# Performance work log

Measured on AMD Instinct MI355X. Metric: run time of the kernel, lower is better.

## Reference

```python
import jax, jax.numpy as jnp
import numpy as np

B, S, E, D, H = 4, 2048, 512, 64, 8
NEG = float(np.finfo(np.float64).min)  # tf uses tf.float64.min; overflows to -inf in fp32, same softmax effect


def setup_inputs() -> dict:
    key = jax.random.key(0)
    ks = jax.random.split(key, 6)
    std = 0.05  # tf.random_normal_initializer default stddev
    x = jax.random.normal(ks[0], (B, S, E), dtype=jnp.float32)
    Wq = jax.random.normal(ks[1], (H, E, D), dtype=jnp.float32) * std
    Wk = jax.random.normal(ks[2], (H, E, D), dtype=jnp.float32) * std
    Wvd = jax.random.normal(ks[3], (H, E, D), dtype=jnp.float32) * std
    Wvu = jax.random.normal(ks[4], (H, D, E), dtype=jnp.float32) * std
    Wo = jax.random.normal(ks[5], (H, 1), dtype=jnp.float32) * std
    return {"x": x, "Wq": Wq, "Wk": Wk, "Wvd": Wvd, "Wvu": Wvu, "Wo": Wo}


def reference(x, Wq, Wk, Wvd, Wvu, Wo):
    # Per-head projections, vectorized over the head axis h
    Q = jnp.einsum("bse,hed->bhsd", x, Wq)  # [B,H,S,D]
    K = jnp.einsum("bse,hed->bhsd", x, Wk)
    score = jnp.einsum("bhsd,bhtd->bhst", Q, K) / jnp.sqrt(jnp.float32(D))
    # tf.linalg.band_part(score, -1, 0): keep lower triangle (causal)
    tril = jnp.tril(jnp.ones((S, S), dtype=bool))
    score = jnp.where(tril, score, 0.0)
    # tf.where(score != 0, score, float64.min): masks zeros (incl. any exact-zero kept entries)
    score = jnp.where(score != 0, score, jnp.float32(NEG))
    attn = jax.nn.softmax(score, axis=-1)  # [B,H,S,S]
    # low-rank value projection: x @ (Wvdown @ Wvup) per head
    Wv = jnp.einsum("hed,hdf->hef", Wvd, Wvu)  # [H,E,E]
    V = jnp.einsum("bse,hef->bhsf", x, Wv)      # [B,H,S,E]
    heads = jnp.einsum("bhst,bhte->bhse", attn, V)  # [B,H,S,E]
    # stack on last axis then matmul with Wo[H,1] == weighted sum over heads
    out = jnp.einsum("bhse,h->bse", heads, Wo[:, 0])
    return out
```

## Files before the change

### kernel.cpp

```cpp
#include <hip/hip_runtime.h>
#include <math.h>
#include <type_traits>

namespace {
constexpr int B = 4, S = 2048, E = 512, D = 64, H = 8;
constexpr int KD = 512;

typedef short bf8 __attribute__((ext_vector_type(8)));
typedef short bf4 __attribute__((ext_vector_type(4)));
typedef float f4 __attribute__((ext_vector_type(4)));

__device__ __forceinline__ short f2bf(float f) {
  union { float f; unsigned u; } v; v.f = f;
  const unsigned r = v.u + 0x7fffu + ((v.u >> 16) & 1u);
  return (short)(r >> 16);
}

__device__ __forceinline__ unsigned cvt_pk_bf16(float a, float b) {
  unsigned r;
  asm("v_cvt_pk_bf16_f32 %0, %1, %2" : "=v"(r) : "v"(a), "v"(b));
  return r;
}

__device__ __forceinline__ void gload16(const void* g, void* l) {
  __builtin_amdgcn_global_load_lds(
      (const __attribute__((address_space(1))) unsigned int*)g,
      (__attribute__((address_space(3))) unsigned int*)l, 16, 0, 0);
}

__global__ __launch_bounds__(256) void prep_kernel(
    const float* __restrict__ x, const float* __restrict__ Wq,
    const float* __restrict__ Wk, const float* __restrict__ Wvd,
    const float* __restrict__ Wvu, const float* __restrict__ Wo,
    short* __restrict__ xb, short* __restrict__ WcatT,
    short* __restrict__ W2T) {
  __shared__ float T[64][65];
  const int bid = blockIdx.x;
  const int tid = threadIdx.x;
  if (bid < 2048) {
    const size_t i = ((size_t)bid * 256 + tid) * 8;
    const float4 v0 = *(const float4*)(x + i);
    const float4 v1 = *(const float4*)(x + i + 4);
    bf8 o;
    o[0] = f2bf(v0.x); o[1] = f2bf(v0.y); o[2] = f2bf(v0.z); o[3] = f2bf(v0.w);
    o[4] = f2bf(v1.x); o[5] = f2bf(v1.y); o[6] = f2bf(v1.z); o[7] = f2bf(v1.w);
    *(bf8*)(xb + i) = o;
  } else if (bid < 2240) {
    const int r = bid - 2048;
    const int cb = r >> 3, e0 = (r & 7) * 64;
    const int w = cb >> 3, h = cb & 7;
    const float* Wsel = (w == 0) ? Wq : (w == 1) ? Wk : Wvd;
    const float* Wp = Wsel + (size_t)h * E * D;
#pragma unroll
    for (int i = 0; i < 4; ++i) {
      const int f = tid + i * 256;
      const int rr = f >> 4, c4 = f & 15;
      const float4 v = *(const float4*)(Wp + (size_t)(e0 + rr) * D + c4 * 4);
      T[rr][c4 * 4 + 0] = v.x; T[rr][c4 * 4 + 1] = v.y;
      T[rr][c4 * 4 + 2] = v.z; T[rr][c4 * 4 + 3] = v.w;
    }
    __syncthreads();
#pragma unroll
    for (int i = 0; i < 4; ++i) {
      const int f = tid + i * 256;
      const int dr = f >> 4, e4 = f & 15;
      bf4 o;
#pragma unroll
      for (int j = 0; j < 4; ++j) o[j] = f2bf(T[e4 * 4 + j][dr]);
      *(bf4*)(WcatT + (size_t)(cb * 64 + dr) * KD + e0 + e4 * 4) = o;
    }
  } else {
    const int r = bid - 2240;
    const int h = r >> 3, e0 = (r & 7) * 64;
    const float wo = Wo[h];
#pragma unroll
    for (int i = 0; i < 4; ++i) {
      const int f = tid + i * 256;
      const int rr = f >> 4, c4 = f & 15;
      const float4 v = *(const float4*)(Wvu + ((size_t)h * D + rr) * E + e0 + c4 * 4);
      T[rr][c4 * 4 + 0] = v.x * wo; T[rr][c4 * 4 + 1] = v.y * wo;
      T[rr][c4 * 4 + 2] = v.z * wo; T[rr][c4 * 4 + 3] = v.w * wo;
    }
    __syncthreads();
#pragma unroll
    for (int i = 0; i < 4; ++i) {
      const int f = tid + i * 256;
      const int er = f >> 4, d4 = f & 15;
      bf4 o;
#pragma unroll
      for (int j = 0; j < 4; ++j) o[j] = f2bf(T[d4 * 4 + j][er]);
      *(bf4*)(W2T + (size_t)(e0 + er) * KD + h * 64 + d4 * 4) = o;
    }
  }
}

template <int MODE>
__global__ __launch_bounds__(256) void gemm_kernel(
    const short* __restrict__ A, const short* __restrict__ Bt,
    short* __restrict__ Qb, short* __restrict__ Kb, short* __restrict__ Vtg,
    float* __restrict__ Of) {
  const int row0 = blockIdx.x * 128;
  const int ct = blockIdx.y;
  const int tid = threadIdx.x;
  const int w = tid >> 6, l = tid & 63;
  const int wm = w >> 1, wn = w & 1;
  const int lr = l & 15, hi = l >> 4;

  __shared__ short As[128 * 64];
  __shared__ short Bs[128 * 64];

  const short* Ag = A + (size_t)row0 * KD;
  const short* Bg = Bt + (size_t)ct * 128 * KD;

  f4 acc[4][4] = {};
  for (int k0 = 0; k0 < KD; k0 += 64) {
    __syncthreads();
#pragma unroll
    for (int i = 0; i < 4; ++i) {
      const int f = i * 256 + tid;
      const int r = f >> 3, g = f & 7;
      gload16(Ag + (size_t)r * KD + k0 + ((g ^ (r & 7)) << 3), &As[f * 8]);
    }
#pragma unroll
    for (int i = 0; i < 4; ++i) {
      const int f = i * 256 + tid;
      const int r = f >> 3, g = f & 7;
      gload16(Bg + (size_t)r * KD + k0 + ((g ^ (r & 7)) << 3), &Bs[f * 8]);
    }
    __syncthreads();

    bf8 af[4][2], bfv[4][2];
#pragma unroll
    for (int t = 0; t < 4; ++t) {
#pragma unroll
      for (int kh = 0; kh < 2; ++kh) {
        const int ar = wm * 64 + t * 16 + lr;
        af[t][kh] = *(const bf8*)&As[ar * 64 + (((kh * 4 + hi) ^ (ar & 7)) << 3)];
        const int br = wn * 64 + t * 16 + lr;
        bfv[t][kh] = *(const bf8*)&Bs[br * 64 + (((kh * 4 + hi) ^ (br & 7)) << 3)];
      }
    }
#pragma unroll
    for (int mt = 0; mt < 4; ++mt)
#pragma unroll
      for (int nt = 0; nt < 4; ++nt) {
        acc[mt][nt] =
            __builtin_amdgcn_mfma_f32_16x16x32_bf16(af[mt][0], bfv[nt][0], acc[mt][nt], 0, 0, 0);
        acc[mt][nt] =
            __builtin_amdgcn_mfma_f32_16x16x32_bf16(af[mt][1], bfv[nt][1], acc[mt][nt], 0, 0, 0);
      }
  }

  if constexpr (MODE == 0) {
#pragma unroll
    for (int nt = 0; nt < 4; ++nt) {
      const int gc = ct * 128 + wn * 64 + nt * 16 + lr;
      const int cb = gc >> 6, d = gc & 63;
      const int h = cb & 7;
      if (cb < 16) {
        short* Out = (cb < 8) ? Qb : Kb;
#pragma unroll
        for (int mt = 0; mt < 4; ++mt)
#pragma unroll
          for (int reg = 0; reg < 4; ++reg) {
            const int grow = row0 + wm * 64 + mt * 16 + hi * 4 + reg;
            const int b = grow >> 11, s = grow & (S - 1);
            Out[(((size_t)(b * H + h) * S + s) << 6) + d] = f2bf(acc[mt][nt][reg]);
          }
      } else {
        const int hswap = ((d >> 3) & 1) << 2;
#pragma unroll
        for (int mt = 0; mt < 4; ++mt) {
          const int grow0 = row0 + wm * 64 + mt * 16 + hi * 4;
          const int b = grow0 >> 11, s0 = (grow0 & (S - 1)) ^ hswap;
          bf4 o;
#pragma unroll
          for (int reg = 0; reg < 4; ++reg) o[reg] = f2bf(acc[mt][nt][reg]);
          *(bf4*)(Vtg + (((size_t)(b * H + h) * D + d) << 11) + s0) = o;
        }
      }
    }
  } else {
#pragma unroll
    for (int mt = 0; mt < 4; ++mt)
#pragma unroll
      for (int reg = 0; reg < 4; ++reg) {
        const int grow = row0 + wm * 64 + mt * 16 + hi * 4 + reg;
        float* orow = Of + (size_t)grow * 512 + ct * 128 + wn * 64;
#pragma unroll
        for (int nt = 0; nt < 4; ++nt) orow[nt * 16 + lr] = acc[mt][nt][reg];
      }
  }
}

__global__ __launch_bounds__(256) void attn_kernel(
    const short* __restrict__ Qb, const short* __restrict__ Kb,
    const short* __restrict__ Vt, short* __restrict__ PVb) {
  const int bh = blockIdx.x;
  const int j = blockIdx.y;
  const int qtA = j, qtB = 31 - j;
  const int nA = j + 1;
  const int b = bh >> 3, h = bh & 7;
  const int tid = threadIdx.x;
  const int w = tid >> 6, l = tid & 63;
  const int lr = l & 15, hi = l >> 4;

  __shared__ short Ks[2][64 * 64];
  __shared__ short Vs[2][64 * 64];

  const short* QgA = Qb + ((size_t)bh * S + qtA * 64 + w * 16 + lr) * D;
  const short* QgB = Qb + ((size_t)bh * S + qtB * 64 + w * 16 + lr) * D;
  const bf8 qA0 = *(const bf8*)(QgA + hi * 8);
  const bf8 qA1 = *(const bf8*)(QgA + 32 + hi * 8);
  const bf8 qB0 = *(const bf8*)(QgB + hi * 8);
  const bf8 qB1 = *(const bf8*)(QgB + 32 + hi * 8);

  const short* Kg = Kb + (size_t)bh * S * D;
  const short* Vg = Vt + (size_t)bh * D * S;

  const int sr = tid >> 3, sg = tid & 7;
  const int sswz = (sg ^ (sr & 7)) << 3;
  const int sr2 = sr + 32, sswz2 = (sg ^ (sr2 & 7)) << 3;
  const short* kg0 = Kg + (size_t)sr * D + sswz;
  const short* kg1 = Kg + (size_t)sr2 * D + sswz2;
  const short* vg0 = Vg + (size_t)sr * S + sswz;
  const short* vg1 = Vg + (size_t)sr2 * S + sswz2;

  const int e7 = lr & 7;
  const int kla0 = lr * 128 + ((hi ^ e7) << 4);
  const int kla1 = kla0 ^ 64;
  const int x7 = (hi >> 1) ^ e7;
  const int swaph = ((hi & 1) ^ ((lr >> 3) & 1)) << 3;
  int vla[4];
#pragma unroll
  for (int np = 0; np < 4; ++np)
    vla[np] = lr * 128 + (((2 * np) ^ x7) << 4) + swaph;

  float lsum4[4] = {};
  f4 accO[4] = {};

  auto step = [&](int buf, bf8 q0, bf8 q1, auto diag_c) {
    constexpr bool DIAG = decltype(diag_c)::value;
    const char* Klb = (const char*)Ks[buf];
    const char* Vlb = (const char*)Vs[buf];
    f4 accS[4] = {};
    __builtin_amdgcn_s_setprio(1);
#pragma unroll
    for (int n = 0; n < 4; ++n) {
      const bf8 k0 = *(const bf8*)(Klb + kla0 + n * 2048);
      const bf8 k1 = *(const bf8*)(Klb + kla1 + n * 2048);
      accS[n] = __builtin_amdgcn_mfma_f32_16x16x32_bf16(k0, q0, accS[n], 0, 0, 0);
      accS[n] = __builtin_amdgcn_mfma_f32_16x16x32_bf16(k1, q1, accS[n], 0, 0, 0);
    }
    __builtin_amdgcn_s_setprio(0);

    bf4 pa[4];
#pragma unroll
    for (int n = 0; n < 4; ++n) {
      float p[4];
#pragma unroll
      for (int reg = 0; reg < 4; ++reg) {
        float pv = __expf(fmaf(accS[n][reg], 0.125f, -12.0f));
        if constexpr (DIAG) {
          const bool ok = (n * 16 + hi * 4 + reg) <= (w * 16 + lr);
          pv = ok ? pv : 0.f;
        }
        p[reg] = pv;
        lsum4[reg] += pv;
      }
      union { int2 i; bf4 v; } u;
      u.i.x = (int)cvt_pk_bf16(p[0], p[1]);
      u.i.y = (int)cvt_pk_bf16(p[2], p[3]);
      pa[n] = u.v;
    }

    __builtin_amdgcn_s_setprio(1);
#pragma unroll
    for (int np = 0; np < 4; ++np) {
#pragma unroll
      for (int ne = 0; ne < 4; ++ne) {
        const bf4 vf = *(const bf4*)(Vlb + vla[np] + ne * 2048);
        accO[ne] = __builtin_amdgcn_mfma_f32_16x16x16bf16_1k(pa[np], vf, accO[ne], 0, 0, 0);
      }
    }
    __builtin_amdgcn_s_setprio(0);
  };

  auto epi = [&](int qt) {
    float lv = (lsum4[0] + lsum4[1]) + (lsum4[2] + lsum4[3]);
    lv += __shfl_xor(lv, 16);
    lv += __shfl_xor(lv, 32);
#pragma unroll
    for (int reg = 0; reg < 4; ++reg) {
      const float lq = __shfl(lv, hi * 4 + reg);
      const float inv = 1.f / lq;
      const int s = qt * 64 + w * 16 + hi * 4 + reg;
      short* op = PVb + (size_t)(b * S + s) * (H * D) + h * D;
#pragma unroll
      for (int n = 0; n < 4; ++n) op[n * 16 + lr] = f2bf(accO[n][reg] * inv);
    }
  };

  gload16(kg0, &Ks[0][tid * 8]);
  gload16(kg1, &Ks[0][(256 + tid) * 8]);
  gload16(vg0, &Vs[0][tid * 8]);
  gload16(vg1, &Vs[0][(256 + tid) * 8]);

  int buf = 0;
  for (int s = 0; s < 33; ++s) {
    if (s > 0) {
      __builtin_amdgcn_s_barrier();
      __builtin_amdgcn_sched_barrier(0);
    }
    if (s < 32) {
      const int ktn = (s + 1 < nA) ? s + 1 : s + 1 - nA;
      const size_t ko = (size_t)ktn << 12;
      const size_t vo = (size_t)ktn << 6;
      const int nb = buf ^ 1;
      gload16(kg0 + ko, &Ks[nb][tid * 8]);
      gload16(kg1 + ko, &Ks[nb][(256 + tid) * 8]);
      gload16(vg0 + vo, &Vs[nb][tid * 8]);
      gload16(vg1 + vo, &Vs[nb][(256 + tid) * 8]);
      asm volatile("s_waitcnt vmcnt(4)" ::: "memory");
    } else {
      asm volatile("s_waitcnt vmcnt(0)" ::: "memory");
    }
    __builtin_amdgcn_sched_barrier(0);
    __builtin_amdgcn_s_barrier();
    __builtin_amdgcn_sched_barrier(0);

    if (s < nA) {
      if (s == nA - 1) step(buf, qA0, qA1, std::true_type{});
      else             step(buf, qA0, qA1, std::false_type{});
    } else {
      if (s == 32)     step(buf, qB0, qB1, std::true_type{});
      else             step(buf, qB0, qB1, std::false_type{});
    }

    if (s == nA - 1) {
      epi(qtA);
#pragma unroll
      for (int n = 0; n < 4; ++n) accO[n] = f4{0.f, 0.f, 0.f, 0.f};
      lsum4[0] = lsum4[1] = lsum4[2] = lsum4[3] = 0.f;
    }
    buf ^= 1;
  }
  epi(qtB);
}

}

extern "C" void kernel_launch(void* const* d_in, const int* in_sizes, int n_in,
                              void* d_out, int out_size, void* d_ws, size_t ws_size,
                              hipStream_t stream) {
  const float* x   = (const float*)d_in[0];
  const float* Wq  = (const float*)d_in[1];
  const float* Wk  = (const float*)d_in[2];
  const float* Wvd = (const float*)d_in[3];
  const float* Wvu = (const float*)d_in[4];
  const float* Wo  = (const float*)d_in[5];
  float* out = (float*)d_out;

  const size_t nqk = (size_t)B * H * S * D;
  short* xb    = (short*)d_ws;
  short* Qb    = xb + nqk;
  short* Kb    = Qb + nqk;
  short* Vtg   = Kb + nqk;
  short* PVb   = Vtg + nqk;
  short* WcatT = PVb + nqk;
  short* W2T   = WcatT + 1536 * KD;

  prep_kernel<<<dim3(2304), 256, 0, stream>>>(x, Wq, Wk, Wvd, Wvu, Wo,
                                              xb, WcatT, W2T);
  gemm_kernel<0><<<dim3(64, 12), 256, 0, stream>>>(xb, WcatT, Qb, Kb, Vtg, nullptr);
  attn_kernel<<<dim3(B * H, 16), 256, 0, stream>>>(Qb, Kb, Vtg, PVb);
  gemm_kernel<1><<<dim3(64, 4), 256, 0, stream>>>(PVb, W2T, nullptr, nullptr, nullptr, out);
}
```

Measured before the change: 81.05 us.

## Process two KV chunks per barrier with four-deep LDS ring buffer

Replaces the double-buffered K/V pipeline in the attention kernel with a 4-slot LDS ring. Each iteration handles two 64-key chunks and prefetches the next two, which halves the number of block barriers and deepens prefetch. In exchange LDS use doubles to 64KB per block, which may lower occupancy, and the code size grows from duplicated step bodies.

Result: slower. 82.98 us (+2.4%).

```diff
diff --git a/kernel.cpp b/kernel.cpp
--- a/kernel.cpp
+++ b/kernel.cpp
@@ -205,8 +205,8 @@
   const int w = tid >> 6, l = tid & 63;
   const int lr = l & 15, hi = l >> 4;
 
-  __shared__ short Ks[2][64 * 64];
-  __shared__ short Vs[2][64 * 64];
+  __shared__ short Ks[4][64 * 64];
+  __shared__ short Vs[4][64 * 64];
 
   const short* QgA = Qb + ((size_t)bh * S + qtA * 64 + w * 16 + lr) * D;
   const short* QgB = Qb + ((size_t)bh * S + qtB * 64 + w * 16 + lr) * D;
@@ -301,26 +301,50 @@
     }
   };
 
-  gload16(kg0, &Ks[0][tid * 8]);
-  gload16(kg1, &Ks[0][(256 + tid) * 8]);
-  gload16(vg0, &Vs[0][tid * 8]);
-  gload16(vg1, &Vs[0][(256 + tid) * 8]);
-
-  int buf = 0;
-  for (int s = 0; s < 33; ++s) {
+  auto issue_chunk = [&](int c) {
+    const int kt = (c < nA) ? c : c - nA;
+    const size_t ko = (size_t)kt << 12;
+    const size_t vo = (size_t)kt << 6;
+    const int bb = c & 3;
+    gload16(kg0 + ko, &Ks[bb][tid * 8]);
+    gload16(kg1 + ko, &Ks[bb][(256 + tid) * 8]);
+    gload16(vg0 + vo, &Vs[bb][tid * 8]);
+    gload16(vg1 + vo, &Vs[bb][(256 + tid) * 8]);
+  };
+
+  auto do_chunk = [&](int c) {
+    const int bb = c & 3;
+    if (c < nA) {
+      if (c == nA - 1) {
+        step(bb, qA0, qA1, std::true_type{});
+        epi(qtA);
+#pragma unroll
+        for (int n = 0; n < 4; ++n) accO[n] = f4{0.f, 0.f, 0.f, 0.f};
+        lsum4[0] = lsum4[1] = lsum4[2] = lsum4[3] = 0.f;
+      } else {
+        step(bb, qA0, qA1, std::false_type{});
+      }
+    } else {
+      if (c == 32) step(bb, qB0, qB1, std::true_type{});
+      else         step(bb, qB0, qB1, std::false_type{});
+    }
+  };
+
+  issue_chunk(0);
+  issue_chunk(1);
+
+  for (int s = 0; s < 17; ++s) {
     if (s > 0) {
       __builtin_amdgcn_s_barrier();
       __builtin_amdgcn_sched_barrier(0);
     }
-    if (s < 32) {
-      const int ktn = (s + 1 < nA) ? s + 1 : s + 1 - nA;
-      const size_t ko = (size_t)ktn << 12;
-      const size_t vo = (size_t)ktn << 6;
-      const int nb = buf ^ 1;
-      gload16(kg0 + ko, &Ks[nb][tid * 8]);
-      gload16(kg1 + ko, &Ks[nb][(256 + tid) * 8]);
-      gload16(vg0 + vo, &Vs[nb][tid * 8]);
-      gload16(vg1 + vo, &Vs[nb][(256 + tid) * 8]);
+    const int c0 = 2 * s, c1 = c0 + 1;
+    const int p0 = c0 + 2, p1 = c0 + 3;
+    if (p0 < 33) issue_chunk(p0);
+    if (p1 < 33) issue_chunk(p1);
+    if (p1 < 33) {
+      asm volatile("s_waitcnt vmcnt(8)" ::: "memory");
+    } else if (p0 < 33) {
       asm volatile("s_waitcnt vmcnt(4)" ::: "memory");
     } else {
       asm volatile("s_waitcnt vmcnt(0)" ::: "memory");
@@ -329,21 +353,8 @@
     __builtin_amdgcn_s_barrier();
     __builtin_amdgcn_sched_barrier(0);
 
-    if (s < nA) {
-      if (s == nA - 1) step(buf, qA0, qA1, std::true_type{});
-      else             step(buf, qA0, qA1, std::false_type{});
-    } else {
-      if (s == 32)     step(buf, qB0, qB1, std::true_type{});
-      else             step(buf, qB0, qB1, std::false_type{});
-    }
-
-    if (s == nA - 1) {
-      epi(qtA);
-#pragma unroll
-      for (int n = 0; n < 4; ++n) accO[n] = f4{0.f, 0.f, 0.f, 0.f};
-      lsum4[0] = lsum4[1] = lsum4[2] = lsum4[3] = 0.f;
-    }
-    buf ^= 1;
+    do_chunk(c0);
+    if (c1 < 33) do_chunk(c1);
   }
   epi(qtB);
 }
```
